# Performance work log

Hardware: AMD Instinct MI355X
Metric: run time of the kernel (lower is better)

## Reference

```python
import jax, jax.numpy as jnp
import numpy as np

B, T, D, OUT = 128, 4096, 64, 512  # batch(list len), max frames, feature_size, output_size


def setup_inputs() -> dict:
    key = jax.random.key(0)
    ks = jax.random.split(key, 12)
    s = 0.05
    return {
        "x": jax.random.normal(ks[0], (B, T, D), jnp.float32),
        # true frame counts per ragged item, in [256, T]
        "lengths": jax.random.randint(ks[1], (B,), 256, T + 1, dtype=jnp.int32),
        # td1: Conv2d(1, D, (3, D)) weight [D,1,3,D], bias [D]
        "W1": jax.random.normal(ks[2], (D, 1, 3, D), jnp.float32) * s,
        "b1": jax.random.normal(ks[3], (D,), jnp.float32) * s,
        # td2: Conv2d(1, D, (1, D)) weight [D,1,1,D], bias [D]
        "W2": jax.random.normal(ks[4], (D, 1, 1, D), jnp.float32) * s,
        "b2": jax.random.normal(ks[5], (D,), jnp.float32) * s,
        # segment-level MLP: D->256->256->OUT (torch Linear layout [out,in])
        "Wl1": jax.random.normal(ks[6], (256, D), jnp.float32) * s,
        "bl1": jax.random.normal(ks[7], (256,), jnp.float32) * s,
        "Wl2": jax.random.normal(ks[8], (256, 256), jnp.float32) * s,
        "bl2": jax.random.normal(ks[9], (256,), jnp.float32) * s,
        "Wl3": jax.random.normal(ks[10], (OUT, 256), jnp.float32) * s,
        "bl3": jax.random.normal(ks[11], (OUT,), jnp.float32) * s,
    }


def reference(x, lengths, W1, b1, W2, b2, Wl1, bl1, Wl2, bl2, Wl3, bl3):
    # td1: sliding window of 3 frames, full-width feature contraction -> [B, T-2, F]
    # (avoid materializing [B,T-2,3,D] windows; 3 shifted matmuls instead)
    w1 = W1[:, 0]  # [F, 3, D]
    h = b1
    for k in range(3):  # fixed tiny kernel width
        h = h + jnp.einsum('btd,fd->btf', x[:, k:T - 2 + k], w1[:, k])
    h = jax.nn.relu(h)
    # td2: context 0 -> per-frame linear F->F
    h = jnp.einsum('btf,gf->btg', h, W2[:, 0, 0]) + b2  # [B, T-2, F]
    # masked mean over valid frames (each item has lengths[i]-2 conv outputs)
    nvalid = (lengths - 2).astype(h.dtype)  # [B]
    mask = (jnp.arange(T - 2)[None, :] < (lengths - 2)[:, None]).astype(h.dtype)
    pooled = jnp.einsum('btg,bt->bg', h, mask) / nvalid[:, None]  # [B, F]
    # segment-level MLP
    z = jax.nn.relu(pooled @ Wl1.T + bl1)
    z = jax.nn.relu(z @ Wl2.T + bl2)
    return z @ Wl3.T + bl3  # [B, OUT]
```

## Files before the change

### kernel.cpp

```cpp
#include <hip/hip_runtime.h>
#include <hip/hip_bf16.h>

#define NB 128
#define NT 4096
#define ND 64
#define CH 128
#define NCHUNK 32
#define NSEGS 33

typedef __attribute__((ext_vector_type(8))) short bf16x8;
typedef __attribute__((ext_vector_type(4))) float f32x4;

__device__ __forceinline__ short bfb(float f) {
    __hip_bfloat16 h = __float2bfloat16(f);
    return __builtin_bit_cast(short, h);
}

__device__ __forceinline__ bf16x8 pack8(f32x4 a, f32x4 b) {
    bf16x8 r;
    r[0] = bfb(a[0]); r[1] = bfb(a[1]); r[2] = bfb(a[2]); r[3] = bfb(a[3]);
    r[4] = bfb(b[0]); r[5] = bfb(b[1]); r[6] = bfb(b[2]); r[7] = bfb(b[3]);
    return r;
}

__global__ void setup_kernel(const float* __restrict__ W1, short* __restrict__ wb) {
    int idx = blockIdx.x * 256 + threadIdx.x;
    if (idx >= 4 * 6 * 64) return;
    int lane = idx & 63;
    int kk   = (idx >> 6) % 6;
    int nt   = idx / (6 * 64);
    const float* wp = W1 + (nt * 16 + (lane & 15)) * 192 + (lane >> 4) * 8 + kk * 32;
    bf16x8 r;
    #pragma unroll
    for (int j = 0; j < 8; ++j) r[j] = bfb(wp[j]);
    reinterpret_cast<bf16x8*>(wb)[idx] = r;
}

__global__ __launch_bounds__(256) void conv_pool_kernel(
    const float* __restrict__ x, const int* __restrict__ lengths,
    const short* __restrict__ wb, const float* __restrict__ b1,
    float* __restrict__ s_sum)
{
    __shared__ float lds[NSEGS * 256];
    __shared__ float sh_red[4 * 64];

    const int b      = blockIdx.x >> 5;
    const int chunk  = blockIdx.x & (NCHUNK - 1);
    const int nvalid = lengths[b] - 2;
    const int t0     = chunk * CH;
    if (t0 >= nvalid) return;

    const int lane = threadIdx.x & 63;
    const int wave = threadIdx.x >> 6;
    const int lrow = lane & 15;
    const int lkg  = lane >> 4;

    const int rows_needed = min(CH + 2, nvalid - t0 + 2);
    const float* xb = x + (size_t)b * (NT * ND);

    {
        const int unit = lane & 15;
        const int rl4  = lane >> 4;
        for (int s = wave; s < NSEGS; s += 4) {
            if (s * 4 < rows_needed) {
                int row_local = s * 4 + rl4;
                int rg = t0 + row_local; if (rg > NT - 1) rg = NT - 1;
                int su = unit ^ (row_local & 7);
                const float* src = xb + (size_t)rg * ND + su * 4;
                __builtin_amdgcn_global_load_lds(
                    (const __attribute__((address_space(1))) void*)src,
                    (__attribute__((address_space(3))) void*)&lds[s * 256],
                    16, 0, 0);
            }
        }
    }

    bf16x8 wfrag[4][6];
    #pragma unroll
    for (int nt = 0; nt < 4; ++nt)
        #pragma unroll
        for (int kk = 0; kk < 6; ++kk)
            wfrag[nt][kk] = reinterpret_cast<const bf16x8*>(wb)[(nt * 6 + kk) * 64 + lane];
    float b1f[4];
    #pragma unroll
    for (int nt = 0; nt < 4; ++nt) b1f[nt] = b1[nt * 16 + lrow];

    __syncthreads();

    float sums[4] = {0.f, 0.f, 0.f, 0.f};

    #pragma unroll
    for (int i = 0; i < 2; ++i) {
        const int tile = wave + i * 4;
        const int tl0  = tile * 16;
        if (t0 + tl0 < nvalid) {
            f32x4 acc[4];
            #pragma unroll
            for (int nt = 0; nt < 4; ++nt) acc[nt] = (f32x4){0.f, 0.f, 0.f, 0.f};

            #pragma unroll
            for (int kk = 0; kk < 6; ++kk) {
                const int xrl = tl0 + lrow + (kk >> 1);
                const int e   = lkg * 2 + (kk & 1) * 8;
                const int sw  = xrl & 7;
                f32x4 a0 = *reinterpret_cast<const f32x4*>(&lds[xrl * 64 + ((e ^ sw) << 2)]);
                f32x4 a1 = *reinterpret_cast<const f32x4*>(&lds[xrl * 64 + (((e + 1) ^ sw) << 2)]);
                bf16x8 afrag = pack8(a0, a1);
                #pragma unroll
                for (int nt = 0; nt < 4; ++nt)
                    acc[nt] = __builtin_amdgcn_mfma_f32_16x16x32_bf16(
                        afrag, wfrag[nt][kk], acc[nt], 0, 0, 0);
            }

            #pragma unroll
            for (int r = 0; r < 4; ++r) {
                const bool valid = (t0 + tl0 + lkg * 4 + r) < nvalid;
                #pragma unroll
                for (int nt = 0; nt < 4; ++nt) {
                    float v = fmaxf(acc[nt][r] + b1f[nt], 0.f);
                    if (valid) sums[nt] += v;
                }
            }
        }
    }

    #pragma unroll
    for (int nt = 0; nt < 4; ++nt) {
        float v = sums[nt];
        v += __shfl_xor(v, 16, 64);
        v += __shfl_xor(v, 32, 64);
        if (lane < 16) sh_red[wave * 64 + nt * 16 + lane] = v;
    }
    __syncthreads();
    if (threadIdx.x < 64) {
        float tot = sh_red[threadIdx.x] + sh_red[64 + threadIdx.x] +
                    sh_red[128 + threadIdx.x] + sh_red[192 + threadIdx.x];
        atomicAdd(&s_sum[b * 64 + threadIdx.x], tot);
    }
}

__global__ __launch_bounds__(256) void mlp_kernel(
    const float* __restrict__ s_sum, const int* __restrict__ lengths,
    const float* __restrict__ W2, const float* __restrict__ b2,
    const float* __restrict__ Wl1, const float* __restrict__ bl1,
    const float* __restrict__ Wl2, const float* __restrict__ bl2,
    const float* __restrict__ Wl3, const float* __restrict__ bl3,
    float* __restrict__ out)
{
    __shared__ float sh_s[64], sh_p[64], sh_z1[256], sh_z2[256];
    const int b = blockIdx.x, tid = threadIdx.x;

    if (tid < 64)
        sh_s[tid] = s_sum[b * 64 + tid] / (float)(lengths[b] - 2);
    __syncthreads();

    if (tid < 64) {
        f32x4 acc = {0.f, 0.f, 0.f, 0.f};
        const f32x4* wr = reinterpret_cast<const f32x4*>(W2 + tid * 64);
        const f32x4* vr = reinterpret_cast<const f32x4*>(sh_s);
        #pragma unroll
        for (int k = 0; k < 16; ++k) acc += wr[k] * vr[k];
        sh_p[tid] = b2[tid] + acc[0] + acc[1] + acc[2] + acc[3];
    }
    __syncthreads();

    {
        f32x4 acc = {0.f, 0.f, 0.f, 0.f};
        const f32x4* wr = reinterpret_cast<const f32x4*>(Wl1 + tid * 64);
        const f32x4* vr = reinterpret_cast<const f32x4*>(sh_p);
        #pragma unroll
        for (int k = 0; k < 16; ++k) acc += wr[k] * vr[k];
        sh_z1[tid] = fmaxf(bl1[tid] + acc[0] + acc[1] + acc[2] + acc[3], 0.f);
    }
    __syncthreads();

    {
        f32x4 a0 = {0.f, 0.f, 0.f, 0.f}, a1 = {0.f, 0.f, 0.f, 0.f};
        const f32x4* wr = reinterpret_cast<const f32x4*>(Wl2 + tid * 256);
        const f32x4* vr = reinterpret_cast<const f32x4*>(sh_z1);
        #pragma unroll
        for (int k = 0; k < 64; k += 2) { a0 += wr[k] * vr[k]; a1 += wr[k + 1] * vr[k + 1]; }
        f32x4 a = a0 + a1;
        sh_z2[tid] = fmaxf(bl2[tid] + a[0] + a[1] + a[2] + a[3], 0.f);
    }
    __syncthreads();

    {
        f32x4 a0 = {0.f, 0.f, 0.f, 0.f}, a1 = {0.f, 0.f, 0.f, 0.f};
        const f32x4* w0 = reinterpret_cast<const f32x4*>(Wl3 + (size_t)tid * 256);
        const f32x4* w1 = reinterpret_cast<const f32x4*>(Wl3 + (size_t)(tid + 256) * 256);
        const f32x4* vr = reinterpret_cast<const f32x4*>(sh_z2);
        #pragma unroll
        for (int k = 0; k < 64; ++k) { a0 += w0[k] * vr[k]; a1 += w1[k] * vr[k]; }
        out[(size_t)b * 512 + tid]       = bl3[tid]       + a0[0] + a0[1] + a0[2] + a0[3];
        out[(size_t)b * 512 + 256 + tid] = bl3[tid + 256] + a1[0] + a1[1] + a1[2] + a1[3];
    }
}

extern "C" void kernel_launch(void* const* d_in, const int* in_sizes, int n_in,
                              void* d_out, int out_size, void* d_ws, size_t ws_size,
                              hipStream_t stream) {
    const float* x       = (const float*)d_in[0];
    const int*   lengths = (const int*)d_in[1];
    const float* W1      = (const float*)d_in[2];
    const float* b1      = (const float*)d_in[3];
    const float* W2      = (const float*)d_in[4];
    const float* b2      = (const float*)d_in[5];
    const float* Wl1     = (const float*)d_in[6];
    const float* bl1     = (const float*)d_in[7];
    const float* Wl2     = (const float*)d_in[8];
    const float* bl2     = (const float*)d_in[9];
    const float* Wl3     = (const float*)d_in[10];
    const float* bl3     = (const float*)d_in[11];
    float* out = (float*)d_out;

    float* s_sum = (float*)d_ws;
    short* wb    = (short*)((char*)d_ws + NB * ND * 4);

    hipMemsetAsync(s_sum, 0, NB * ND * sizeof(float), stream);
    setup_kernel<<<dim3(6), dim3(256), 0, stream>>>(W1, wb);
    conv_pool_kernel<<<dim3(NB * NCHUNK), dim3(256), 0, stream>>>(x, lengths, wb, b1, s_sum);
    mlp_kernel<<<dim3(NB), dim3(256), 0, stream>>>(s_sum, lengths, W2, b2,
                                                   Wl1, bl1, Wl2, bl2, Wl3, bl3, out);
}
```

Before: 245.5 us.

## Per-wave LDS staging, partial-sum slots instead of atomics, transposed MLP weights

Each wave now loads its own 32+4 frame rows into a private LDS region and waits only on its own loads, so the block-wide barrier before compute goes away. Chunk results are written to per-chunk slots rather than atomically added, which removes the memset. The MLP kernel reduces those slots and reads pre-transposed weights so neighbouring threads load contiguous addresses. The cost is a larger prep kernel that transposes all MLP weights on every call, somewhat more LDS (overlapping halo rows per wave), and W1 fragments read from global memory inside the MFMA loop instead of being held in registers.

```diff
diff --git a/kernel.cpp b/kernel.cpp
--- a/kernel.cpp
+++ b/kernel.cpp
@@ -6,7 +6,6 @@
 #define ND 64
 #define CH 128
 #define NCHUNK 32
-#define NSEGS 33
 
 typedef __attribute__((ext_vector_type(8))) short bf16x8;
 typedef __attribute__((ext_vector_type(4))) float f32x4;
@@ -23,98 +22,127 @@
     return r;
 }
 
-__global__ void setup_kernel(const float* __restrict__ W1, short* __restrict__ wb) {
+#define OFF_SPART 0
+#define OFF_WB    (1048576)
+#define OFF_W2T   (OFF_WB + 32768)
+#define OFF_WL1T  (OFF_W2T + 16384)
+#define OFF_WL2T  (OFF_WL1T + 65536)
+#define OFF_WL3T  (OFF_WL2T + 262144)
+
+#define N_WB   1536
+#define N_W2T  4096
+#define N_WL1T 16384
+#define N_WL2T 65536
+#define N_WL3T 131072
+#define PREP_TOTAL (N_WB + N_W2T + N_WL1T + N_WL2T + N_WL3T)
+
+__global__ __launch_bounds__(256) void prep_kernel(
+    const float* __restrict__ W1, const float* __restrict__ W2,
+    const float* __restrict__ Wl1, const float* __restrict__ Wl2,
+    const float* __restrict__ Wl3,
+    short* __restrict__ wb, float* __restrict__ W2T, float* __restrict__ Wl1T,
+    float* __restrict__ Wl2T, float* __restrict__ Wl3T)
+{
     int idx = blockIdx.x * 256 + threadIdx.x;
-    if (idx >= 4 * 6 * 64) return;
-    int lane = idx & 63;
-    int kk   = (idx >> 6) % 6;
-    int nt   = idx / (6 * 64);
-    const float* wp = W1 + (nt * 16 + (lane & 15)) * 192 + (lane >> 4) * 8 + kk * 32;
-    bf16x8 r;
-    #pragma unroll
-    for (int j = 0; j < 8; ++j) r[j] = bfb(wp[j]);
-    reinterpret_cast<bf16x8*>(wb)[idx] = r;
+    if (idx < N_WB) {
+        int lane = idx & 63;
+        int kk   = (idx >> 6) % 6;
+        int nt   = idx / (6 * 64);
+        const float* wp = W1 + (nt * 16 + (lane & 15)) * 192 + (lane >> 4) * 8 + kk * 32;
+        bf16x8 r;
+        #pragma unroll
+        for (int j = 0; j < 8; ++j) r[j] = bfb(wp[j]);
+        reinterpret_cast<bf16x8*>(wb)[idx] = r;
+        return;
+    }
+    idx -= N_WB;
+    if (idx < N_W2T)  { W2T[idx]  = W2[(idx & 63) * 64 + (idx >> 6)]; return; }
+    idx -= N_W2T;
+    if (idx < N_WL1T) { Wl1T[idx] = Wl1[(idx & 255) * 64 + (idx >> 8)]; return; }
+    idx -= N_WL1T;
+    if (idx < N_WL2T) { Wl2T[idx] = Wl2[(idx & 255) * 256 + (idx >> 8)]; return; }
+    idx -= N_WL2T;
+    if (idx < N_WL3T) { Wl3T[idx] = Wl3[(idx & 511) * 256 + (idx >> 9)]; return; }
 }
 
 __global__ __launch_bounds__(256) void conv_pool_kernel(
     const float* __restrict__ x, const int* __restrict__ lengths,
     const short* __restrict__ wb, const float* __restrict__ b1,
-    float* __restrict__ s_sum)
+    float* __restrict__ s_part)
 {
-    __shared__ float lds[NSEGS * 256];
-    __shared__ float sh_red[4 * 64];
+    __shared__ float lds[4 * 36 * 64];
+    __shared__ float sh_red[256];
 
     const int b      = blockIdx.x >> 5;
     const int chunk  = blockIdx.x & (NCHUNK - 1);
     const int nvalid = lengths[b] - 2;
     const int t0     = chunk * CH;
-    if (t0 >= nvalid) return;
+    float* slot = s_part + ((size_t)b * NCHUNK + chunk) * 64;
+    if (t0 >= nvalid) {
+        if (threadIdx.x < 64) slot[threadIdx.x] = 0.f;
+        return;
+    }
 
     const int lane = threadIdx.x & 63;
     const int wave = threadIdx.x >> 6;
     const int lrow = lane & 15;
     const int lkg  = lane >> 4;
 
-    const int rows_needed = min(CH + 2, nvalid - t0 + 2);
     const float* xb = x + (size_t)b * (NT * ND);
-
-    {
+    const int tbase = t0 + wave * 32;
+    const bool t0v = tbase < nvalid;
+    const bool t1v = (tbase + 16) < nvalid;
+    float* ldsw = &lds[wave * (36 * 64)];
+
+    if (t0v) {
+        const int nsegs = t1v ? 9 : 5;
+        const int jl   = lane >> 4;
         const int unit = lane & 15;
-        const int rl4  = lane >> 4;
-        for (int s = wave; s < NSEGS; s += 4) {
-            if (s * 4 < rows_needed) {
-                int row_local = s * 4 + rl4;
-                int rg = t0 + row_local; if (rg > NT - 1) rg = NT - 1;
-                int su = unit ^ (row_local & 7);
-                const float* src = xb + (size_t)rg * ND + su * 4;
-                __builtin_amdgcn_global_load_lds(
-                    (const __attribute__((address_space(1))) void*)src,
-                    (__attribute__((address_space(3))) void*)&lds[s * 256],
-                    16, 0, 0);
-            }
+        for (int s = 0; s < nsegs; ++s) {
+            const int j  = s * 4 + jl;
+            int rg = tbase + j; if (rg > NT - 1) rg = NT - 1;
+            const int su = unit ^ (j & 7);
+            const float* src = xb + (size_t)rg * ND + su * 4;
+            __builtin_amdgcn_global_load_lds(
+                (const __attribute__((address_space(1))) void*)src,
+                (__attribute__((address_space(3))) void*)&ldsw[s * 256],
+                16, 0, 0);
         }
     }
 
-    bf16x8 wfrag[4][6];
-    #pragma unroll
-    for (int nt = 0; nt < 4; ++nt)
-        #pragma unroll
-        for (int kk = 0; kk < 6; ++kk)
-            wfrag[nt][kk] = reinterpret_cast<const bf16x8*>(wb)[(nt * 6 + kk) * 64 + lane];
     float b1f[4];
     #pragma unroll
     for (int nt = 0; nt < 4; ++nt) b1f[nt] = b1[nt * 16 + lrow];
 
-    __syncthreads();
-
+    asm volatile("s_waitcnt vmcnt(0)" ::: "memory");
+
+    const bf16x8* wb8 = reinterpret_cast<const bf16x8*>(wb);
     float sums[4] = {0.f, 0.f, 0.f, 0.f};
 
     #pragma unroll
     for (int i = 0; i < 2; ++i) {
-        const int tile = wave + i * 4;
-        const int tl0  = tile * 16;
-        if (t0 + tl0 < nvalid) {
+        if (i == 0 ? t0v : t1v) {
             f32x4 acc[4];
             #pragma unroll
             for (int nt = 0; nt < 4; ++nt) acc[nt] = (f32x4){0.f, 0.f, 0.f, 0.f};
 
             #pragma unroll
             for (int kk = 0; kk < 6; ++kk) {
-                const int xrl = tl0 + lrow + (kk >> 1);
-                const int e   = lkg * 2 + (kk & 1) * 8;
-                const int sw  = xrl & 7;
-                f32x4 a0 = *reinterpret_cast<const f32x4*>(&lds[xrl * 64 + ((e ^ sw) << 2)]);
-                f32x4 a1 = *reinterpret_cast<const f32x4*>(&lds[xrl * 64 + (((e + 1) ^ sw) << 2)]);
-                bf16x8 afrag = pack8(a0, a1);
+                const int j  = i * 16 + lrow + (kk >> 1);
+                const int e  = lkg * 2 + (kk & 1) * 8;
+                const int sw = j & 7;
+                f32x4 a0 = *reinterpret_cast<const f32x4*>(&ldsw[j * 64 + ((e ^ sw) << 2)]);
+                f32x4 a1 = *reinterpret_cast<const f32x4*>(&ldsw[j * 64 + (((e + 1) ^ sw) << 2)]);
+                bf16x8 af = pack8(a0, a1);
                 #pragma unroll
                 for (int nt = 0; nt < 4; ++nt)
                     acc[nt] = __builtin_amdgcn_mfma_f32_16x16x32_bf16(
-                        afrag, wfrag[nt][kk], acc[nt], 0, 0, 0);
+                        af, wb8[(nt * 6 + kk) * 64 + lane], acc[nt], 0, 0, 0);
             }
 
             #pragma unroll
             for (int r = 0; r < 4; ++r) {
-                const bool valid = (t0 + tl0 + lkg * 4 + r) < nvalid;
+                const bool valid = (tbase + i * 16 + lkg * 4 + r) < nvalid;
                 #pragma unroll
                 for (int nt = 0; nt < 4; ++nt) {
                     float v = fmaxf(acc[nt][r] + b1f[nt], 0.f);
@@ -132,68 +160,70 @@
         if (lane < 16) sh_red[wave * 64 + nt * 16 + lane] = v;
     }
     __syncthreads();
-    if (threadIdx.x < 64) {
-        float tot = sh_red[threadIdx.x] + sh_red[64 + threadIdx.x] +
-                    sh_red[128 + threadIdx.x] + sh_red[192 + threadIdx.x];
-        atomicAdd(&s_sum[b * 64 + threadIdx.x], tot);
-    }
+    if (threadIdx.x < 64)
+        slot[threadIdx.x] = sh_red[threadIdx.x] + sh_red[64 + threadIdx.x] +
+                            sh_red[128 + threadIdx.x] + sh_red[192 + threadIdx.x];
 }
 
 __global__ __launch_bounds__(256) void mlp_kernel(
-    const float* __restrict__ s_sum, const int* __restrict__ lengths,
-    const float* __restrict__ W2, const float* __restrict__ b2,
-    const float* __restrict__ Wl1, const float* __restrict__ bl1,
-    const float* __restrict__ Wl2, const float* __restrict__ bl2,
-    const float* __restrict__ Wl3, const float* __restrict__ bl3,
+    const float* __restrict__ s_part, const int* __restrict__ lengths,
+    const float* __restrict__ W2T, const float* __restrict__ b2,
+    const float* __restrict__ Wl1T, const float* __restrict__ bl1,
+    const float* __restrict__ Wl2T, const float* __restrict__ bl2,
+    const float* __restrict__ Wl3T, const float* __restrict__ bl3,
     float* __restrict__ out)
 {
-    __shared__ float sh_s[64], sh_p[64], sh_z1[256], sh_z2[256];
+    __shared__ float sh_r[256], sh_s[64], sh_p[64], sh_z1[256], sh_z2[256];
     const int b = blockIdx.x, tid = threadIdx.x;
 
+    {
+        const int f = tid & 63, c0 = tid >> 6;
+        const float* sp = s_part + (size_t)b * NCHUNK * 64;
+        float p = 0.f;
+        #pragma unroll
+        for (int c = 0; c < 8; ++c) p += sp[(c0 + c * 4) * 64 + f];
+        sh_r[tid] = p;
+    }
+    __syncthreads();
     if (tid < 64)
-        sh_s[tid] = s_sum[b * 64 + tid] / (float)(lengths[b] - 2);
+        sh_s[tid] = (sh_r[tid] + sh_r[64 + tid] + sh_r[128 + tid] + sh_r[192 + tid])
+                    / (float)(lengths[b] - 2);
     __syncthreads();
 
     if (tid < 64) {
-        f32x4 acc = {0.f, 0.f, 0.f, 0.f};
-        const f32x4* wr = reinterpret_cast<const f32x4*>(W2 + tid * 64);
-        const f32x4* vr = reinterpret_cast<const f32x4*>(sh_s);
-        #pragma unroll
-        for (int k = 0; k < 16; ++k) acc += wr[k] * vr[k];
-        sh_p[tid] = b2[tid] + acc[0] + acc[1] + acc[2] + acc[3];
-    }
-    __syncthreads();
-
-    {
-        f32x4 acc = {0.f, 0.f, 0.f, 0.f};
-        const f32x4* wr = reinterpret_cast<const f32x4*>(Wl1 + tid * 64);
-        const f32x4* vr = reinterpret_cast<const f32x4*>(sh_p);
-        #pragma unroll
-        for (int k = 0; k < 16; ++k) acc += wr[k] * vr[k];
-        sh_z1[tid] = fmaxf(bl1[tid] + acc[0] + acc[1] + acc[2] + acc[3], 0.f);
-    }
-    __syncthreads();
-
-    {
-        f32x4 a0 = {0.f, 0.f, 0.f, 0.f}, a1 = {0.f, 0.f, 0.f, 0.f};
-        const f32x4* wr = reinterpret_cast<const f32x4*>(Wl2 + tid * 256);
-        const f32x4* vr = reinterpret_cast<const f32x4*>(sh_z1);
-        #pragma unroll
-        for (int k = 0; k < 64; k += 2) { a0 += wr[k] * vr[k]; a1 += wr[k + 1] * vr[k + 1]; }
-        f32x4 a = a0 + a1;
-        sh_z2[tid] = fmaxf(bl2[tid] + a[0] + a[1] + a[2] + a[3], 0.f);
-    }
-    __syncthreads();
-
-    {
-        f32x4 a0 = {0.f, 0.f, 0.f, 0.f}, a1 = {0.f, 0.f, 0.f, 0.f};
-        const f32x4* w0 = reinterpret_cast<const f32x4*>(Wl3 + (size_t)tid * 256);
-        const f32x4* w1 = reinterpret_cast<const f32x4*>(Wl3 + (size_t)(tid + 256) * 256);
-        const f32x4* vr = reinterpret_cast<const f32x4*>(sh_z2);
-        #pragma unroll
-        for (int k = 0; k < 64; ++k) { a0 += w0[k] * vr[k]; a1 += w1[k] * vr[k]; }
-        out[(size_t)b * 512 + tid]       = bl3[tid]       + a0[0] + a0[1] + a0[2] + a0[3];
-        out[(size_t)b * 512 + 256 + tid] = bl3[tid + 256] + a1[0] + a1[1] + a1[2] + a1[3];
+        float acc = b2[tid];
+        #pragma unroll 8
+        for (int f = 0; f < 64; ++f) acc = fmaf(W2T[f * 64 + tid], sh_s[f], acc);
+        sh_p[tid] = acc;
+    }
+    __syncthreads();
+
+    {
+        float acc = bl1[tid];
+        #pragma unroll 8
+        for (int f = 0; f < 64; ++f) acc = fmaf(Wl1T[f * 256 + tid], sh_p[f], acc);
+        sh_z1[tid] = fmaxf(acc, 0.f);
+    }
+    __syncthreads();
+
+    {
+        float acc = bl2[tid];
+        #pragma unroll 8
+        for (int k = 0; k < 256; ++k) acc = fmaf(Wl2T[k * 256 + tid], sh_z1[k], acc);
+        sh_z2[tid] = fmaxf(acc, 0.f);
+    }
+    __syncthreads();
+
+    {
+        float a0 = bl3[tid], a1 = bl3[tid + 256];
+        #pragma unroll 8
+        for (int k = 0; k < 256; ++k) {
+            const float z = sh_z2[k];
+            a0 = fmaf(Wl3T[k * 512 + tid],       z, a0);
+            a1 = fmaf(Wl3T[k * 512 + tid + 256], z, a1);
+        }
+        out[(size_t)b * 512 + tid]       = a0;
+        out[(size_t)b * 512 + 256 + tid] = a1;
     }
 }
 
@@ -214,12 +244,18 @@
     const float* bl3     = (const float*)d_in[11];
     float* out = (float*)d_out;
 
-    float* s_sum = (float*)d_ws;
-    short* wb    = (short*)((char*)d_ws + NB * ND * 4);
-
-    hipMemsetAsync(s_sum, 0, NB * ND * sizeof(float), stream);
-    setup_kernel<<<dim3(6), dim3(256), 0, stream>>>(W1, wb);
-    conv_pool_kernel<<<dim3(NB * NCHUNK), dim3(256), 0, stream>>>(x, lengths, wb, b1, s_sum);
-    mlp_kernel<<<dim3(NB), dim3(256), 0, stream>>>(s_sum, lengths, W2, b2,
-                                                   Wl1, bl1, Wl2, bl2, Wl3, bl3, out);
-}
+    char* ws = (char*)d_ws;
+    float* s_part = (float*)(ws + OFF_SPART);
+    short* wb     = (short*)(ws + OFF_WB);
+    float* W2T    = (float*)(ws + OFF_W2T);
+    float* Wl1T   = (float*)(ws + OFF_WL1T);
+    float* Wl2T   = (float*)(ws + OFF_WL2T);
+    float* Wl3T   = (float*)(ws + OFF_WL3T);
+
+    prep_kernel<<<dim3((PREP_TOTAL + 255) / 256), dim3(256), 0, stream>>>(
+        W1, W2, Wl1, Wl2, Wl3, wb, W2T, Wl1T, Wl2T, Wl3T);
+    conv_pool_kernel<<<dim3(NB * NCHUNK), dim3(256), 0, stream>>>(
+        x, lengths, wb, b1, s_part);
+    mlp_kernel<<<dim3(NB), dim3(256), 0, stream>>>(
+        s_part, lengths, W2T, b2, Wl1T, bl1, Wl2T, bl2, Wl3T, bl3, out);
+}
```

After: 247.1 us. Within noise of the previous version (+0.6%).
